# Kernel tuning notes

Hardware: AMD Instinct MI355X
Metric: run time of the kernel (lower is better)

The kernel has to match this reference:

```python
import math
import jax, jax.numpy as jnp
import numpy as np

D_MODEL = 128
NUM_HEADS = 8
FACTOR = 5


def setup_inputs() -> dict:
    key = jax.random.key(0)
    ks = jax.random.split(key, 9)
    B, L, dm = 2, 4096, D_MODEL
    s = 1.0 / math.sqrt(dm)
    return {
        "x": jax.random.normal(ks[0], (B, L, dm), dtype=jnp.float32),
        "Wq": jax.random.normal(ks[1], (dm, dm), dtype=jnp.float32) * s,
        "bq": jnp.zeros((dm,), jnp.float32),
        "Wk": jax.random.normal(ks[2], (dm, dm), dtype=jnp.float32) * s,
        "bk": jnp.zeros((dm,), jnp.float32),
        "Wv": jax.random.normal(ks[3], (dm, dm), dtype=jnp.float32) * s,
        "bv": jnp.zeros((dm,), jnp.float32),
        "Wo": jax.random.normal(ks[4], (dm, dm), dtype=jnp.float32) * s,
        "bo": jnp.zeros((dm,), jnp.float32),
    }


def reference(x, Wq, bq, Wk, bk, Wv, bv, Wo, bo):
    B, L, dm = x.shape
    H = NUM_HEADS
    D = dm // H
    inv_sqrt_d = 1.0 / math.sqrt(D)

    def split_heads(t):  # [B,L,dm] -> [B,H,L,D]
        return t.reshape(B, L, H, D).transpose(0, 2, 1, 3)

    Q = split_heads(x @ Wq + bq)
    K = split_heads(x @ Wk + bk)
    V = split_heads(x @ Wv + bv)

    # sample_k = min(L_K, int(log(L_K) * factor)); L is static under jit
    sample_k = min(L, int(math.log(L) * FACTOR))

    # _prob_QK: full scores, per-query stable exp, mean over queries, top-k keys
    scores_full = jnp.einsum("bhqd,bhkd->bhqk", Q, K) * inv_sqrt_d  # [B,H,L,L]
    m = jnp.max(scores_full, axis=-1, keepdims=True)
    e = jnp.exp(scores_full - m)
    mean_attn = jnp.mean(e, axis=2)  # [B,H,L_K]
    _, idx = jax.lax.top_k(mean_attn, sample_k)  # [B,H,sample_k]

    # gather sampled keys/values along the key axis
    Ks = jnp.take_along_axis(K, idx[..., None], axis=2)  # [B,H,s,D]
    Vs = jnp.take_along_axis(V, idx[..., None], axis=2)

    attn = jax.nn.softmax(jnp.einsum("bhqd,bhsd->bhqs", Q, Ks) * inv_sqrt_d, axis=-1)
    out = jnp.einsum("bhqs,bhsd->bhqd", attn, Vs)  # [B,H,L,D]
    out = out.transpose(0, 2, 1, 3).reshape(B, L, dm)
    return out @ Wo + bo
```

## Files before the change

### kernel.cpp

```cpp
#include <hip/hip_runtime.h>
#include <hip/hip_bf16.h>

#define L 4096
#define DM 128
#define NH 8
#define HD 16
#define NBH 16
#define SK 41
#define NSPLIT 8
#define SLICE (L/NSPLIT)
#define KK (SLICE/16)
#define QSCALE 0.36067376022224085f

typedef __attribute__((ext_vector_type(8))) short s16x8;
typedef __attribute__((ext_vector_type(4))) float f32x4;

__device__ __forceinline__ float bf2f(unsigned short h){ return __uint_as_float(((unsigned)h)<<16); }
__device__ __forceinline__ unsigned short f2bf(float f){
  unsigned u = __float_as_uint(f);
  u += 0x7FFFu + ((u>>16)&1u);
  return (unsigned short)(u>>16);
}
__device__ __forceinline__ float fast_exp2(float x){
  float r;
  asm("v_exp_f32 %0, %1" : "=v"(r) : "v"(x));
  return r;
}

__global__ __launch_bounds__(256) void prep(
    const float* __restrict__ x,
    const float* __restrict__ Wq, const float* __restrict__ Wk,
    const float* __restrict__ Wv, const float* __restrict__ Wo,
    unsigned short* __restrict__ Xh, unsigned short* __restrict__ Xl,
    unsigned short* __restrict__ Wph, unsigned short* __restrict__ Wpl)
{
  const int t = threadIdx.x;
  const int blk = blockIdx.x;
  if (blk < 1024){
    const long base = (long)blk*1024 + t*4;
    float4 v = *(const float4*)(x + base);
    unsigned short h[4], lo[4];
    h[0]=f2bf(v.x); lo[0]=f2bf(v.x - bf2f(h[0]));
    h[1]=f2bf(v.y); lo[1]=f2bf(v.y - bf2f(h[1]));
    h[2]=f2bf(v.z); lo[2]=f2bf(v.z - bf2f(h[2]));
    h[3]=f2bf(v.w); lo[3]=f2bf(v.w - bf2f(h[3]));
    *(uint2*)(Xh+base) = *(uint2*)h;
    *(uint2*)(Xl+base) = *(uint2*)lo;
  } else {
    const int e = (blk-1024)*256 + t;
    const int p = e >> 14;
    const int idx = e & 16383;
    const int j = idx & 7;
    const int f = idx >> 3;
    const int n = f & 127;
    const int kcg = f >> 7;
    const int k = (kcg>>1)*16 + (kcg&1)*8 + j;
    const float* W = (p==0)?Wq:((p==1)?Wk:((p==2)?Wv:Wo));
    const float v = W[k*128 + n];
    const unsigned short h = f2bf(v);
    Wph[e] = h;
    Wpl[e] = f2bf(v - bf2f(h));
  }
}

__global__ __launch_bounds__(256) void proj_mfma(
    const unsigned short* __restrict__ Xh, const unsigned short* __restrict__ Xl,
    const unsigned short* __restrict__ Wph, const unsigned short* __restrict__ Wpl,
    const float* __restrict__ bq, const float* __restrict__ bk, const float* __restrict__ bv,
    unsigned short* __restrict__ Qh, unsigned short* __restrict__ Ql,
    unsigned short* __restrict__ Kh, unsigned short* __restrict__ Kl,
    float* __restrict__ Vo)
{
  const int p = blockIdx.y;
  const float* __restrict__ bias = (p==0)?bq:((p==1)?bk:bv);
  __shared__ __align__(16) unsigned short wh[16384];
  __shared__ __align__(16) unsigned short wl[16384];
  const int t = threadIdx.x;
  {
    const uint4* gh = (const uint4*)(Wph + (long)p*16384);
    const uint4* gl = (const uint4*)(Wpl + (long)p*16384);
    uint4* sh = (uint4*)wh; uint4* sl = (uint4*)wl;
#pragma unroll
    for (int i=0;i<8;++i){ sh[t + i*256] = gh[t + i*256]; sl[t + i*256] = gl[t + i*256]; }
  }
  __syncthreads();
  const int w = t>>6, l = t&63;
  const int lc = l&15, g = l>>4;
  const int mbase = blockIdx.x*128 + w*32;
  f32x4 acc[2][8];
#pragma unroll
  for (int mt=0;mt<2;++mt)
#pragma unroll
    for (int nt=0;nt<8;++nt){ acc[mt][nt][0]=0.f; acc[mt][nt][1]=0.f; acc[mt][nt][2]=0.f; acc[mt][nt][3]=0.f; }
  const unsigned short* __restrict__ Asrc = (g<2)? Xh : Xl;
  const int koff = (g&1)*8;
  for (int kc=0; kc<8; ++kc){
    s16x8 a[2];
#pragma unroll
    for (int mt=0;mt<2;++mt)
      a[mt] = *(const s16x8*)(Asrc + ((long)(mbase + mt*16 + lc))*128 + kc*16 + koff);
#pragma unroll
    for (int nt=0;nt<8;++nt){
      const int fi = (kc*2+(g&1))*128 + nt*16 + lc;
      s16x8 b1 = ((const s16x8*)wh)[fi];
      s16x8 b2 = ((const s16x8*)wl)[fi];
#pragma unroll
      for (int mt=0;mt<2;++mt){
        acc[mt][nt] = __builtin_amdgcn_mfma_f32_16x16x32_bf16(a[mt], b1, acc[mt][nt], 0,0,0);
        acc[mt][nt] = __builtin_amdgcn_mfma_f32_16x16x32_bf16(a[mt], b2, acc[mt][nt], 0,0,0);
      }
    }
  }
#pragma unroll
  for (int nt=0;nt<8;++nt){
    const float bb = bias[nt*16 + lc];
#pragma unroll
    for (int mt=0;mt<2;++mt){
#pragma unroll
      for (int r=0;r<4;++r){
        const int row = mbase + mt*16 + g*4 + r;
        float v = acc[mt][nt][r] + bb;
        const int b = row>>12, li = row&4095;
        const long o = (((long)(b*NH + nt))*L + li)*HD + lc;
        if (p==2){
          Vo[o] = v;
        } else {
          if (p==0) v *= QSCALE;
          const unsigned short h = f2bf(v);
          const unsigned short lo2 = f2bf(v - bf2f(h));
          if (p==0){ Qh[o]=h; Ql[o]=lo2; } else { Kh[o]=h; Kl[o]=lo2; }
        }
      }
    }
  }
}

__global__ __launch_bounds__(256) void rowmax_k(
    const unsigned short* __restrict__ Qh, const unsigned short* __restrict__ Ql,
    const unsigned short* __restrict__ Kh, const unsigned short* __restrict__ Kl,
    float* __restrict__ mpart)
{
  const int bh = blockIdx.y, qt = blockIdx.x, ks = blockIdx.z;
  const int t = threadIdx.x, w = t>>6, l = t&63;
  const int half = (l>>4)&1, part = l>>5, lc = l&15;
  s16x8 aq[4];
  {
    const unsigned short* Qsrc = part ? Ql : Qh;
#pragma unroll
    for (int m=0;m<4;++m){
      const int row = qt*256 + w*64 + m*16 + lc;
      aq[m] = *(const s16x8*)(Qsrc + (((long)bh*L + row)*HD) + half*8);
    }
  }
  f32x4 fz; fz[0]=0.f; fz[1]=0.f; fz[2]=0.f; fz[3]=0.f;
  f32x4 rmax[4];
#pragma unroll
  for (int m=0;m<4;++m){ rmax[m][0]=rmax[m][1]=rmax[m][2]=rmax[m][3]=-3.4e38f; }
  const unsigned short* khp = Kh + ((long)bh*L + ks*SLICE + lc)*HD + half*8;
  const unsigned short* klp = Kl + ((long)bh*L + ks*SLICE + lc)*HD + half*8;
  s16x8 A1 = *(const s16x8*)khp;
  s16x8 A2 = *(const s16x8*)klp;
  for (int kk=0; kk<KK; kk+=2){
    s16x8 B1 = *(const s16x8*)(khp + (kk+1)*256);
    s16x8 B2 = *(const s16x8*)(klp + (kk+1)*256);
#pragma unroll
    for (int m=0;m<4;++m){
      f32x4 acc = __builtin_amdgcn_mfma_f32_16x16x32_bf16(aq[m], A2, fz, 0,0,0);
      acc = __builtin_amdgcn_mfma_f32_16x16x32_bf16(aq[m], A1, acc, 0,0,0);
#pragma unroll
      for (int r=0;r<4;++r) rmax[m][r] = fmaxf(rmax[m][r], acc[r]);
    }
    A1 = *(const s16x8*)(khp + (kk+2)*256);
    A2 = *(const s16x8*)(klp + (kk+2)*256);
#pragma unroll
    for (int m=0;m<4;++m){
      f32x4 acc = __builtin_amdgcn_mfma_f32_16x16x32_bf16(aq[m], B2, fz, 0,0,0);
      acc = __builtin_amdgcn_mfma_f32_16x16x32_bf16(aq[m], B1, acc, 0,0,0);
#pragma unroll
      for (int r=0;r<4;++r) rmax[m][r] = fmaxf(rmax[m][r], acc[r]);
    }
  }
#pragma unroll
  for (int m=0;m<4;++m){
#pragma unroll
    for (int r=0;r<4;++r){
      float v = rmax[m][r];
      v = fmaxf(v, __shfl_xor(v, 1));
      v = fmaxf(v, __shfl_xor(v, 2));
      v = fmaxf(v, __shfl_xor(v, 4));
      v = fmaxf(v, __shfl_xor(v, 8));
      rmax[m][r] = v;
    }
  }
  if (lc == 0){
    const int q4 = l>>4;
#pragma unroll
    for (int m=0;m<4;++m){
#pragma unroll
      for (int r=0;r<4;++r){
        const int row = qt*256 + w*64 + m*16 + q4*4 + r;
        mpart[((long)ks*NBH + bh)*L + row] = rmax[m][r];
      }
    }
  }
}

__global__ __launch_bounds__(256) void mreduce(
    const float* __restrict__ mpart, float* __restrict__ wq)
{
  const int i = blockIdx.x*256 + threadIdx.x;
  float m = -3.4e38f;
#pragma unroll
  for (int p=0;p<NSPLIT;++p) m = fmaxf(m, mpart[(long)p*NBH*L + i]);
  wq[i] = fast_exp2(-m);
}

__global__ __launch_bounds__(256) void colexp_k(
    const unsigned short* __restrict__ Kh, const unsigned short* __restrict__ Kl,
    const unsigned short* __restrict__ Qh, const unsigned short* __restrict__ Ql,
    const float* __restrict__ wq, float* __restrict__ cspart)
{
  const int bh = blockIdx.y, kt = blockIdx.x, qs = blockIdx.z;
  const int t = threadIdx.x, w = t>>6, l = t&63;
  const int half = (l>>4)&1, part = l>>5, lc = l&15;
  s16x8 ak[4];
  {
    const unsigned short* Ksrc = part ? Kl : Kh;
#pragma unroll
    for (int m=0;m<4;++m){
      const int key = kt*256 + w*64 + m*16 + lc;
      ak[m] = *(const s16x8*)(Ksrc + (((long)bh*L + key)*HD) + half*8);
    }
  }
  f32x4 fz; fz[0]=0.f; fz[1]=0.f; fz[2]=0.f; fz[3]=0.f;
  f32x4 csum[4];
#pragma unroll
  for (int m=0;m<4;++m){ csum[m][0]=0.f; csum[m][1]=0.f; csum[m][2]=0.f; csum[m][3]=0.f; }
  const unsigned short* qhp = Qh + ((long)bh*L + qs*SLICE + lc)*HD + half*8;
  const unsigned short* qlp = Ql + ((long)bh*L + qs*SLICE + lc)*HD + half*8;
  const float* wg = wq + (long)bh*L + qs*SLICE + lc;
  s16x8 A1 = *(const s16x8*)qhp;
  s16x8 A2 = *(const s16x8*)qlp;
  float WA = wg[0];
  for (int kk=0; kk<KK; kk+=2){
    s16x8 B1 = *(const s16x8*)(qhp + (kk+1)*256);
    s16x8 B2 = *(const s16x8*)(qlp + (kk+1)*256);
    float WB = wg[(kk+1)*16];
#pragma unroll
    for (int m=0;m<4;++m){
      f32x4 acc = __builtin_amdgcn_mfma_f32_16x16x32_bf16(ak[m], A2, fz, 0,0,0);
      acc = __builtin_amdgcn_mfma_f32_16x16x32_bf16(ak[m], A1, acc, 0,0,0);
#pragma unroll
      for (int r=0;r<4;++r)
        csum[m][r] = fmaf(fast_exp2(acc[r]), WA, csum[m][r]);
    }
    A1 = *(const s16x8*)(qhp + (kk+2)*256);
    A2 = *(const s16x8*)(qlp + (kk+2)*256);
    WA = wg[(kk+2)*16];
#pragma unroll
    for (int m=0;m<4;++m){
      f32x4 acc = __builtin_amdgcn_mfma_f32_16x16x32_bf16(ak[m], B2, fz, 0,0,0);
      acc = __builtin_amdgcn_mfma_f32_16x16x32_bf16(ak[m], B1, acc, 0,0,0);
#pragma unroll
      for (int r=0;r<4;++r)
        csum[m][r] = fmaf(fast_exp2(acc[r]), WB, csum[m][r]);
    }
  }
#pragma unroll
  for (int m=0;m<4;++m){
#pragma unroll
    for (int r=0;r<4;++r){
      float v = csum[m][r];
      v += __shfl_xor(v, 1);
      v += __shfl_xor(v, 2);
      v += __shfl_xor(v, 4);
      v += __shfl_xor(v, 8);
      csum[m][r] = v;
    }
  }
  if (lc == 0){
    const int k4 = l>>4;
#pragma unroll
    for (int m=0;m<4;++m){
#pragma unroll
      for (int r=0;r<4;++r){
        const int key = kt*256 + w*64 + m*16 + k4*4 + r;
        cspart[((long)qs*NBH + bh)*L + key] = csum[m][r];
      }
    }
  }
}

__global__ __launch_bounds__(256) void topk_gather(
    const float* __restrict__ cspart,
    const unsigned short* __restrict__ Kh, const unsigned short* __restrict__ Kl,
    const float* __restrict__ V,
    float* __restrict__ Ks, float* __restrict__ Vs)
{
  const int bh = blockIdx.x;
  const int t = threadIdx.x;
  __shared__ float vals[4096];
  __shared__ unsigned hist[2048];
  __shared__ unsigned suf[256];
  __shared__ int meta[4];
  __shared__ int sel[SK];
  __shared__ int sorted[SK];
  __shared__ int tiei[4096];

  for (int i=t; i<1024; i+=256){
    float4 s = {0.f,0.f,0.f,0.f};
#pragma unroll
    for (int p=0;p<NSPLIT;++p){
      float4 v = *(const float4*)(cspart + ((long)p*NBH + bh)*L + i*4);
      s.x += v.x; s.y += v.y; s.z += v.z; s.w += v.w;
    }
    *(float4*)&vals[i*4] = s;
  }
  __syncthreads();

  int target = SK;
  unsigned B1 = 0, P2 = 0, T = 0;
#pragma unroll
  for (int pass=0; pass<3; ++pass){
    const int nb = (pass<2) ? 2048 : 1024;
    const int chunk = nb >> 8;
    for (int i=t;i<nb;i+=256) hist[i]=0u;
    __syncthreads();
    for (int i=t;i<4096;i+=256){
      const unsigned u = __float_as_uint(vals[i]);
      bool ok; int bk;
      if (pass==0){ ok = true;              bk = (int)(u>>21); }
      else if (pass==1){ ok = ((u>>21)==B1); bk = (int)((u>>10)&0x7FFu); }
      else { ok = ((u>>10)==P2);            bk = (int)(u&0x3FFu); }
      if (ok) atomicAdd(&hist[bk], 1u);
    }
    __syncthreads();
    {
      unsigned c=0;
#pragma unroll
      for (int b=0;b<8;++b) if (b<chunk) c += hist[t*chunk+b];
      suf[t]=c;
    }
    __syncthreads();
    for (int off=1; off<256; off<<=1){
      unsigned add = (t+off<256)? suf[t+off] : 0u;
      __syncthreads();
      suf[t] += add;
      __syncthreads();
    }
    {
      const unsigned mysuf = suf[t];
      const unsigned nxt = (t==255)?0u:suf[t+1];
      if (mysuf >= (unsigned)target && nxt < (unsigned)target){
        unsigned running = nxt;
        for (int b=t*chunk+chunk-1; b>=t*chunk; --b){
          const unsigned h = hist[b];
          if (running + h >= (unsigned)target){ meta[0]=b; meta[1]=(int)running; break; }
          running += h;
        }
      }
    }
    __syncthreads();
    const unsigned B = (unsigned)meta[0];
    target -= meta[1];
    if (pass==0) B1 = B;
    else if (pass==1) P2 = (B1<<11)|B;
    else T = (P2<<10)|B;
    __syncthreads();
  }
  if (t==0){ meta[2]=0; meta[3]=0; }
  __syncthreads();
  for (int i=t;i<4096;i+=256){
    const unsigned u = __float_as_uint(vals[i]);
    if (u > T){ int p = atomicAdd(&meta[2],1); sel[p]=i; }
    else if (u == T){ int p = atomicAdd(&meta[3],1); tiei[p]=i; }
  }
  __syncthreads();
  const int ngt = meta[2];
  const int ntie = meta[3];
  for (int j=t; j<ntie; j+=256){
    const int x = tiei[j];
    int rk=0;
    for (int k=0;k<ntie;++k) rk += (tiei[k] < x);
    if (rk < target) sel[ngt+rk] = x;
  }
  __syncthreads();
  if (t<SK){
    int x=sel[t]; int rk=0;
    for (int j=0;j<SK;++j) rk += (sel[j]<x);
    sorted[rk]=x;
  }
  __syncthreads();
  for (int i=t;i<SK*HD;i+=256){
    const int j=i>>4, dd=i&15;
    const int key=sorted[j];
    const long src=((long)bh*L+key)*HD+dd;
    Ks[(long)bh*SK*HD+i]=bf2f(Kh[src])+bf2f(Kl[src]);
    Vs[(long)bh*SK*HD+i]=V[src];
  }
}

__global__ __launch_bounds__(256) void sattn(
    const unsigned short* __restrict__ Qh, const unsigned short* __restrict__ Ql,
    const float* __restrict__ Ks, const float* __restrict__ Vs,
    unsigned short* __restrict__ AOh, unsigned short* __restrict__ AOl)
{
  const int bh = blockIdx.y, qb = blockIdx.x;
  const int t = threadIdx.x;
  __shared__ float ks[SK*HD], vs[SK*HD];
  for (int i=t; i<SK*HD; i+=256){
    ks[i] = Ks[(long)bh*SK*HD + i];
    vs[i] = Vs[(long)bh*SK*HD + i];
  }
  __syncthreads();
  const int q = qb*128 + (t>>1);
  const int half = t&1;
  const long qo = ((long)bh*L + q)*HD;
  float qv[16];
  {
    s16x8 h0 = *(const s16x8*)(Qh+qo);
    s16x8 h1 = *(const s16x8*)(Qh+qo+8);
    s16x8 l0 = *(const s16x8*)(Ql+qo);
    s16x8 l1 = *(const s16x8*)(Ql+qo+8);
#pragma unroll
    for (int d=0; d<8; ++d){
      qv[d]   = bf2f((unsigned short)h0[d]) + bf2f((unsigned short)l0[d]);
      qv[d+8] = bf2f((unsigned short)h1[d]) + bf2f((unsigned short)l1[d]);
    }
  }
  float mrun = -3.4e38f, lrun = 0.f, out[16];
#pragma unroll
  for (int d=0; d<16; ++d) out[d] = 0.f;
  for (int j=half; j<SK; j+=2){
    float4 k0 = *(const float4*)&ks[j*HD+0];
    float4 k1 = *(const float4*)&ks[j*HD+4];
    float4 k2 = *(const float4*)&ks[j*HD+8];
    float4 k3 = *(const float4*)&ks[j*HD+12];
    float s = qv[0]*k0.x;
    s = fmaf(qv[1],k0.y,s); s = fmaf(qv[2],k0.z,s); s = fmaf(qv[3],k0.w,s);
    s = fmaf(qv[4],k1.x,s); s = fmaf(qv[5],k1.y,s); s = fmaf(qv[6],k1.z,s); s = fmaf(qv[7],k1.w,s);
    s = fmaf(qv[8],k2.x,s); s = fmaf(qv[9],k2.y,s); s = fmaf(qv[10],k2.z,s); s = fmaf(qv[11],k2.w,s);
    s = fmaf(qv[12],k3.x,s); s = fmaf(qv[13],k3.y,s); s = fmaf(qv[14],k3.z,s); s = fmaf(qv[15],k3.w,s);
    if (s > mrun){
      const float c = fast_exp2(mrun - s);
      lrun *= c;
#pragma unroll
      for (int d=0; d<16; ++d) out[d] *= c;
      mrun = s;
    }
    const float p = fast_exp2(s - mrun);
    lrun += p;
    float4 v0 = *(const float4*)&vs[j*HD+0];
    float4 v1 = *(const float4*)&vs[j*HD+4];
    float4 v2 = *(const float4*)&vs[j*HD+8];
    float4 v3 = *(const float4*)&vs[j*HD+12];
    out[0]=fmaf(p,v0.x,out[0]); out[1]=fmaf(p,v0.y,out[1]); out[2]=fmaf(p,v0.z,out[2]); out[3]=fmaf(p,v0.w,out[3]);
    out[4]=fmaf(p,v1.x,out[4]); out[5]=fmaf(p,v1.y,out[5]); out[6]=fmaf(p,v1.z,out[6]); out[7]=fmaf(p,v1.w,out[7]);
    out[8]=fmaf(p,v2.x,out[8]); out[9]=fmaf(p,v2.y,out[9]); out[10]=fmaf(p,v2.z,out[10]); out[11]=fmaf(p,v2.w,out[11]);
    out[12]=fmaf(p,v3.x,out[12]); out[13]=fmaf(p,v3.y,out[13]); out[14]=fmaf(p,v3.z,out[14]); out[15]=fmaf(p,v3.w,out[15]);
  }
  const float mo = __shfl_xor(mrun, 1);
  const float lo = __shfl_xor(lrun, 1);
  const float mm = fmaxf(mrun, mo);
  const float cs_ = fast_exp2(mrun - mm);
  const float co_ = fast_exp2(mo - mm);
  const float ltot = fmaf(lrun, cs_, lo*co_);
  const float inv = 1.f / ltot;
#pragma unroll
  for (int d=0; d<16; ++d){
    const float ov = __shfl_xor(out[d], 1);
    out[d] = fmaf(out[d]*cs_, inv, ov*co_*inv);
  }
  if (half == 0){
    const int b = bh>>3, h = bh&7;
    const long row = (long)b*L + q;
    unsigned short hv[16], lv[16];
#pragma unroll
    for (int d=0; d<16; ++d){
      const float v = out[d];
      hv[d] = f2bf(v);
      lv[d] = f2bf(v - bf2f(hv[d]));
    }
    unsigned short* oh = AOh + row*DM + h*HD;
    unsigned short* ol = AOl + row*DM + h*HD;
    *(uint4*)(oh)   = *(uint4*)(hv);
    *(uint4*)(oh+8) = *(uint4*)(hv+8);
    *(uint4*)(ol)   = *(uint4*)(lv);
    *(uint4*)(ol+8) = *(uint4*)(lv+8);
  }
}

__global__ __launch_bounds__(256) void outproj_mfma(
    const unsigned short* __restrict__ AOh, const unsigned short* __restrict__ AOl,
    const unsigned short* __restrict__ Wph, const unsigned short* __restrict__ Wpl,
    const float* __restrict__ bo, float* __restrict__ out)
{
  __shared__ __align__(16) unsigned short wh[16384];
  __shared__ __align__(16) unsigned short wl[16384];
  const int t = threadIdx.x;
  {
    const uint4* gh = (const uint4*)(Wph + (long)3*16384);
    const uint4* gl = (const uint4*)(Wpl + (long)3*16384);
    uint4* sh = (uint4*)wh; uint4* sl = (uint4*)wl;
#pragma unroll
    for (int i=0;i<8;++i){ sh[t + i*256] = gh[t + i*256]; sl[t + i*256] = gl[t + i*256]; }
  }
  __syncthreads();
  const int w = t>>6, l = t&63;
  const int lc = l&15, g = l>>4;
  const int mbase = blockIdx.x*128 + w*32;
  f32x4 acc[2][8];
#pragma unroll
  for (int mt=0;mt<2;++mt)
#pragma unroll
    for (int nt=0;nt<8;++nt){ acc[mt][nt][0]=0.f; acc[mt][nt][1]=0.f; acc[mt][nt][2]=0.f; acc[mt][nt][3]=0.f; }
  const unsigned short* __restrict__ Asrc = (g<2)? AOh : AOl;
  const int koff = (g&1)*8;
  for (int kc=0; kc<8; ++kc){
    s16x8 a[2];
#pragma unroll
    for (int mt=0;mt<2;++mt)
      a[mt] = *(const s16x8*)(Asrc + ((long)(mbase + mt*16 + lc))*128 + kc*16 + koff);
#pragma unroll
    for (int nt=0;nt<8;++nt){
      const int fi = (kc*2+(g&1))*128 + nt*16 + lc;
      s16x8 b1 = ((const s16x8*)wh)[fi];
      s16x8 b2 = ((const s16x8*)wl)[fi];
#pragma unroll
      for (int mt=0;mt<2;++mt){
        acc[mt][nt] = __builtin_amdgcn_mfma_f32_16x16x32_bf16(a[mt], b1, acc[mt][nt], 0,0,0);
        acc[mt][nt] = __builtin_amdgcn_mfma_f32_16x16x32_bf16(a[mt], b2, acc[mt][nt], 0,0,0);
      }
    }
  }
#pragma unroll
  for (int nt=0;nt<8;++nt){
    const float bb = bo[nt*16 + lc];
#pragma unroll
    for (int mt=0;mt<2;++mt){
#pragma unroll
      for (int r=0;r<4;++r){
        const int row = mbase + mt*16 + g*4 + r;
        out[(long)row*DM + nt*16 + lc] = acc[mt][nt][r] + bb;
      }
    }
  }
}

extern "C" void kernel_launch(void* const* d_in, const int* in_sizes, int n_in,
                              void* d_out, int out_size, void* d_ws, size_t ws_size,
                              hipStream_t stream)
{
  const float* x  = (const float*)d_in[0];
  const float* Wq = (const float*)d_in[1];
  const float* bq = (const float*)d_in[2];
  const float* Wk = (const float*)d_in[3];
  const float* bk = (const float*)d_in[4];
  const float* Wv = (const float*)d_in[5];
  const float* bv = (const float*)d_in[6];
  const float* Wo = (const float*)d_in[7];
  const float* bo = (const float*)d_in[8];
  float* out = (float*)d_out;

  char* wsp = (char*)d_ws;
  size_t o = 0;
  auto alloc = [&](size_t bytes)->char*{
    char* p = wsp + o; o += (bytes + 255) & ~(size_t)255; return p;
  };
  unsigned short* Qh = (unsigned short*)alloc((size_t)NBH*L*HD*2);
  unsigned short* Ql = (unsigned short*)alloc((size_t)NBH*L*HD*2);
  unsigned short* Kh = (unsigned short*)alloc((size_t)NBH*L*HD*2);
  unsigned short* Kl = (unsigned short*)alloc((size_t)NBH*L*HD*2);
  float* Vv    = (float*)alloc((size_t)NBH*L*HD*4);
  float* mpart = (float*)alloc((size_t)NSPLIT*NBH*L*4);
  float* cspart= (float*)alloc((size_t)NSPLIT*NBH*L*4);
  float* wqv   = (float*)alloc((size_t)NBH*L*4);
  float* Ks    = (float*)alloc((size_t)NBH*SK*HD*4);
  float* Vs    = (float*)alloc((size_t)NBH*SK*HD*4);
  unsigned short* Xh  = (unsigned short*)alloc((size_t)2*L*DM*2);
  unsigned short* Xl  = (unsigned short*)alloc((size_t)2*L*DM*2);
  unsigned short* AOh = (unsigned short*)alloc((size_t)2*L*DM*2);
  unsigned short* AOl = (unsigned short*)alloc((size_t)2*L*DM*2);
  unsigned short* Wph = (unsigned short*)alloc((size_t)4*16384*2);
  unsigned short* Wpl = (unsigned short*)alloc((size_t)4*16384*2);

  prep<<<1280,256,0,stream>>>(x,Wq,Wk,Wv,Wo,Xh,Xl,Wph,Wpl);
  proj_mfma<<<dim3(64,3),256,0,stream>>>(Xh,Xl,Wph,Wpl,bq,bk,bv,Qh,Ql,Kh,Kl,Vv);
  rowmax_k<<<dim3(16,16,NSPLIT),256,0,stream>>>(Qh,Ql,Kh,Kl,mpart);
  mreduce<<<NBH*L/256,256,0,stream>>>(mpart,wqv);
  colexp_k<<<dim3(16,16,NSPLIT),256,0,stream>>>(Kh,Kl,Qh,Ql,wqv,cspart);
  topk_gather<<<16,256,0,stream>>>(cspart,Kh,Kl,Vv,Ks,Vs);
  sattn<<<dim3(32,16),256,0,stream>>>(Qh,Ql,Ks,Vs,AOh,AOl);
  outproj_mfma<<<64,256,0,stream>>>(AOh,AOl,Wph,Wpl,bo,out);
}
```

Measured before the change: 139.7 us.

## Switch score kernels to 32x32x16 MFMA with three-term split-bf16 products

Rewrites the rowmax and column-exp score kernels to use 32x32x16 bf16 MFMA tiles instead of 16x16x32. Each tile computes hi*hi + lo*hi + hi*lo as three separate MFMAs rather than packing hi/lo into one 32-wide K dimension. This changes the operand layout, register tiling and shuffle reduction, and drops the manual double-buffered prefetch in favour of an unroll-2 loop. The aim is fewer MFMA issues and larger output tiles per wave. The cost is more accumulator registers and possibly less latency hiding of global loads.

```diff
diff --git a/kernel.cpp b/kernel.cpp
--- a/kernel.cpp
+++ b/kernel.cpp
@@ -9,11 +9,12 @@
 #define SK 41
 #define NSPLIT 8
 #define SLICE (L/NSPLIT)
-#define KK (SLICE/16)
+#define NST (SLICE/32)
 #define QSCALE 0.36067376022224085f
 
 typedef __attribute__((ext_vector_type(8))) short s16x8;
 typedef __attribute__((ext_vector_type(4))) float f32x4;
+typedef __attribute__((ext_vector_type(16))) float f32x16;
 
 __device__ __forceinline__ float bf2f(unsigned short h){ return __uint_as_float(((unsigned)h)<<16); }
 __device__ __forceinline__ unsigned short f2bf(float f){
@@ -142,65 +143,50 @@
 {
   const int bh = blockIdx.y, qt = blockIdx.x, ks = blockIdx.z;
   const int t = threadIdx.x, w = t>>6, l = t&63;
-  const int half = (l>>4)&1, part = l>>5, lc = l&15;
-  s16x8 aq[4];
+  const int lk = l&31, ks8 = (l>>5)*8;
+  const int qbase = qt*256 + w*64;
+  s16x8 ah0, al0, ah1, al1;
   {
-    const unsigned short* Qsrc = part ? Ql : Qh;
-#pragma unroll
-    for (int m=0;m<4;++m){
-      const int row = qt*256 + w*64 + m*16 + lc;
-      aq[m] = *(const s16x8*)(Qsrc + (((long)bh*L + row)*HD) + half*8);
-    }
-  }
-  f32x4 fz; fz[0]=0.f; fz[1]=0.f; fz[2]=0.f; fz[3]=0.f;
-  f32x4 rmax[4];
-#pragma unroll
-  for (int m=0;m<4;++m){ rmax[m][0]=rmax[m][1]=rmax[m][2]=rmax[m][3]=-3.4e38f; }
-  const unsigned short* khp = Kh + ((long)bh*L + ks*SLICE + lc)*HD + half*8;
-  const unsigned short* klp = Kl + ((long)bh*L + ks*SLICE + lc)*HD + half*8;
-  s16x8 A1 = *(const s16x8*)khp;
-  s16x8 A2 = *(const s16x8*)klp;
-  for (int kk=0; kk<KK; kk+=2){
-    s16x8 B1 = *(const s16x8*)(khp + (kk+1)*256);
-    s16x8 B2 = *(const s16x8*)(klp + (kk+1)*256);
-#pragma unroll
-    for (int m=0;m<4;++m){
-      f32x4 acc = __builtin_amdgcn_mfma_f32_16x16x32_bf16(aq[m], A2, fz, 0,0,0);
-      acc = __builtin_amdgcn_mfma_f32_16x16x32_bf16(aq[m], A1, acc, 0,0,0);
-#pragma unroll
-      for (int r=0;r<4;++r) rmax[m][r] = fmaxf(rmax[m][r], acc[r]);
-    }
-    A1 = *(const s16x8*)(khp + (kk+2)*256);
-    A2 = *(const s16x8*)(klp + (kk+2)*256);
-#pragma unroll
-    for (int m=0;m<4;++m){
-      f32x4 acc = __builtin_amdgcn_mfma_f32_16x16x32_bf16(aq[m], B2, fz, 0,0,0);
-      acc = __builtin_amdgcn_mfma_f32_16x16x32_bf16(aq[m], B1, acc, 0,0,0);
-#pragma unroll
-      for (int r=0;r<4;++r) rmax[m][r] = fmaxf(rmax[m][r], acc[r]);
-    }
-  }
-#pragma unroll
-  for (int m=0;m<4;++m){
-#pragma unroll
-    for (int r=0;r<4;++r){
-      float v = rmax[m][r];
-      v = fmaxf(v, __shfl_xor(v, 1));
-      v = fmaxf(v, __shfl_xor(v, 2));
-      v = fmaxf(v, __shfl_xor(v, 4));
-      v = fmaxf(v, __shfl_xor(v, 8));
-      rmax[m][r] = v;
-    }
-  }
-  if (lc == 0){
-    const int q4 = l>>4;
-#pragma unroll
-    for (int m=0;m<4;++m){
-#pragma unroll
-      for (int r=0;r<4;++r){
-        const int row = qt*256 + w*64 + m*16 + q4*4 + r;
-        mpart[((long)ks*NBH + bh)*L + row] = rmax[m][r];
-      }
+    const long r0 = ((long)bh*L + qbase + lk)*HD + ks8;
+    ah0 = *(const s16x8*)(Qh + r0);
+    al0 = *(const s16x8*)(Ql + r0);
+    ah1 = *(const s16x8*)(Qh + r0 + 32*HD);
+    al1 = *(const s16x8*)(Ql + r0 + 32*HD);
+  }
+  f32x16 fz, rmax0, rmax1;
+#pragma unroll
+  for (int r=0;r<16;++r){ fz[r]=0.f; rmax0[r]=-3.4e38f; rmax1[r]=-3.4e38f; }
+  const unsigned short* khp = Kh + ((long)bh*L + ks*SLICE + lk)*HD + ks8;
+  const unsigned short* klp = Kl + ((long)bh*L + ks*SLICE + lk)*HD + ks8;
+#pragma unroll 2
+  for (int st=0; st<NST; ++st){
+    s16x8 bhi = *(const s16x8*)(khp + st*32*HD);
+    s16x8 blo = *(const s16x8*)(klp + st*32*HD);
+    f32x16 a0 = __builtin_amdgcn_mfma_f32_32x32x16_bf16(ah0, bhi, fz, 0,0,0);
+    a0 = __builtin_amdgcn_mfma_f32_32x32x16_bf16(al0, bhi, a0, 0,0,0);
+    a0 = __builtin_amdgcn_mfma_f32_32x32x16_bf16(ah0, blo, a0, 0,0,0);
+    f32x16 a1 = __builtin_amdgcn_mfma_f32_32x32x16_bf16(ah1, bhi, fz, 0,0,0);
+    a1 = __builtin_amdgcn_mfma_f32_32x32x16_bf16(al1, bhi, a1, 0,0,0);
+    a1 = __builtin_amdgcn_mfma_f32_32x32x16_bf16(ah1, blo, a1, 0,0,0);
+#pragma unroll
+    for (int r=0;r<16;++r){
+      rmax0[r] = fmaxf(rmax0[r], a0[r]);
+      rmax1[r] = fmaxf(rmax1[r], a1[r]);
+    }
+  }
+  const long obase = ((long)ks*NBH + bh)*L + qbase + 4*(l>>5);
+#pragma unroll
+  for (int r=0;r<16;++r){
+    float v0 = rmax0[r], v1 = rmax1[r];
+    v0 = fmaxf(v0, __shfl_xor(v0,1));  v1 = fmaxf(v1, __shfl_xor(v1,1));
+    v0 = fmaxf(v0, __shfl_xor(v0,2));  v1 = fmaxf(v1, __shfl_xor(v1,2));
+    v0 = fmaxf(v0, __shfl_xor(v0,4));  v1 = fmaxf(v1, __shfl_xor(v1,4));
+    v0 = fmaxf(v0, __shfl_xor(v0,8));  v1 = fmaxf(v1, __shfl_xor(v1,8));
+    v0 = fmaxf(v0, __shfl_xor(v0,16)); v1 = fmaxf(v1, __shfl_xor(v1,16));
+    if (lk == 0){
+      const int rmap = (r&3) + 8*(r>>2);
+      mpart[obase + rmap]      = v0;
+      mpart[obase + 32 + rmap] = v1;
     }
   }
 }
@@ -222,71 +208,52 @@
 {
   const int bh = blockIdx.y, kt = blockIdx.x, qs = blockIdx.z;
   const int t = threadIdx.x, w = t>>6, l = t&63;
-  const int half = (l>>4)&1, part = l>>5, lc = l&15;
-  s16x8 ak[4];
+  const int lk = l&31, ks8 = (l>>5)*8;
+  const int kbase = kt*256 + w*64;
+  s16x8 ah0, al0, ah1, al1;
   {
-    const unsigned short* Ksrc = part ? Kl : Kh;
-#pragma unroll
-    for (int m=0;m<4;++m){
-      const int key = kt*256 + w*64 + m*16 + lc;
-      ak[m] = *(const s16x8*)(Ksrc + (((long)bh*L + key)*HD) + half*8);
-    }
-  }
-  f32x4 fz; fz[0]=0.f; fz[1]=0.f; fz[2]=0.f; fz[3]=0.f;
-  f32x4 csum[4];
-#pragma unroll
-  for (int m=0;m<4;++m){ csum[m][0]=0.f; csum[m][1]=0.f; csum[m][2]=0.f; csum[m][3]=0.f; }
-  const unsigned short* qhp = Qh + ((long)bh*L + qs*SLICE + lc)*HD + half*8;
-  const unsigned short* qlp = Ql + ((long)bh*L + qs*SLICE + lc)*HD + half*8;
-  const float* wg = wq + (long)bh*L + qs*SLICE + lc;
-  s16x8 A1 = *(const s16x8*)qhp;
-  s16x8 A2 = *(const s16x8*)qlp;
-  float WA = wg[0];
-  for (int kk=0; kk<KK; kk+=2){
-    s16x8 B1 = *(const s16x8*)(qhp + (kk+1)*256);
-    s16x8 B2 = *(const s16x8*)(qlp + (kk+1)*256);
-    float WB = wg[(kk+1)*16];
-#pragma unroll
-    for (int m=0;m<4;++m){
-      f32x4 acc = __builtin_amdgcn_mfma_f32_16x16x32_bf16(ak[m], A2, fz, 0,0,0);
-      acc = __builtin_amdgcn_mfma_f32_16x16x32_bf16(ak[m], A1, acc, 0,0,0);
-#pragma unroll
-      for (int r=0;r<4;++r)
-        csum[m][r] = fmaf(fast_exp2(acc[r]), WA, csum[m][r]);
-    }
-    A1 = *(const s16x8*)(qhp + (kk+2)*256);
-    A2 = *(const s16x8*)(qlp + (kk+2)*256);
-    WA = wg[(kk+2)*16];
-#pragma unroll
-    for (int m=0;m<4;++m){
-      f32x4 acc = __builtin_amdgcn_mfma_f32_16x16x32_bf16(ak[m], B2, fz, 0,0,0);
-      acc = __builtin_amdgcn_mfma_f32_16x16x32_bf16(ak[m], B1, acc, 0,0,0);
-#pragma unroll
-      for (int r=0;r<4;++r)
-        csum[m][r] = fmaf(fast_exp2(acc[r]), WB, csum[m][r]);
-    }
-  }
-#pragma unroll
-  for (int m=0;m<4;++m){
-#pragma unroll
-    for (int r=0;r<4;++r){
-      float v = csum[m][r];
-      v += __shfl_xor(v, 1);
-      v += __shfl_xor(v, 2);
-      v += __shfl_xor(v, 4);
-      v += __shfl_xor(v, 8);
-      csum[m][r] = v;
-    }
-  }
-  if (lc == 0){
-    const int k4 = l>>4;
-#pragma unroll
-    for (int m=0;m<4;++m){
-#pragma unroll
-      for (int r=0;r<4;++r){
-        const int key = kt*256 + w*64 + m*16 + k4*4 + r;
-        cspart[((long)qs*NBH + bh)*L + key] = csum[m][r];
-      }
+    const long r0 = ((long)bh*L + kbase + lk)*HD + ks8;
+    ah0 = *(const s16x8*)(Kh + r0);
+    al0 = *(const s16x8*)(Kl + r0);
+    ah1 = *(const s16x8*)(Kh + r0 + 32*HD);
+    al1 = *(const s16x8*)(Kl + r0 + 32*HD);
+  }
+  f32x16 fz, cs0, cs1;
+#pragma unroll
+  for (int r=0;r<16;++r){ fz[r]=0.f; cs0[r]=0.f; cs1[r]=0.f; }
+  const unsigned short* qhp = Qh + ((long)bh*L + qs*SLICE + lk)*HD + ks8;
+  const unsigned short* qlp = Ql + ((long)bh*L + qs*SLICE + lk)*HD + ks8;
+  const float* wgp = wq + (long)bh*L + qs*SLICE + lk;
+#pragma unroll 2
+  for (int st=0; st<NST; ++st){
+    s16x8 bhi = *(const s16x8*)(qhp + st*32*HD);
+    s16x8 blo = *(const s16x8*)(qlp + st*32*HD);
+    const float wv = wgp[st*32];
+    f32x16 a0 = __builtin_amdgcn_mfma_f32_32x32x16_bf16(ah0, bhi, fz, 0,0,0);
+    a0 = __builtin_amdgcn_mfma_f32_32x32x16_bf16(al0, bhi, a0, 0,0,0);
+    a0 = __builtin_amdgcn_mfma_f32_32x32x16_bf16(ah0, blo, a0, 0,0,0);
+    f32x16 a1 = __builtin_amdgcn_mfma_f32_32x32x16_bf16(ah1, bhi, fz, 0,0,0);
+    a1 = __builtin_amdgcn_mfma_f32_32x32x16_bf16(al1, bhi, a1, 0,0,0);
+    a1 = __builtin_amdgcn_mfma_f32_32x32x16_bf16(ah1, blo, a1, 0,0,0);
+#pragma unroll
+    for (int r=0;r<16;++r){
+      cs0[r] = fmaf(fast_exp2(a0[r]), wv, cs0[r]);
+      cs1[r] = fmaf(fast_exp2(a1[r]), wv, cs1[r]);
+    }
+  }
+  const long obase = ((long)qs*NBH + bh)*L + kbase + 4*(l>>5);
+#pragma unroll
+  for (int r=0;r<16;++r){
+    float v0 = cs0[r], v1 = cs1[r];
+    v0 += __shfl_xor(v0,1);  v1 += __shfl_xor(v1,1);
+    v0 += __shfl_xor(v0,2);  v1 += __shfl_xor(v1,2);
+    v0 += __shfl_xor(v0,4);  v1 += __shfl_xor(v1,4);
+    v0 += __shfl_xor(v0,8);  v1 += __shfl_xor(v1,8);
+    v0 += __shfl_xor(v0,16); v1 += __shfl_xor(v1,16);
+    if (lk == 0){
+      const int rmap = (r&3) + 8*(r>>2);
+      cspart[obase + rmap]      = v0;
+      cspart[obase + 32 + rmap] = v1;
     }
   }
 }
```

Measured after the change: 147.8 us. 5.8% more time.
